# Kernel tuning notes

Hardware: AMD Instinct MI355X
Metric: run time of the kernel (lower is better)

Reference implementation:

```python
import jax, jax.numpy as jnp
import numpy as np

B = 65536
QUERY_DIM = 1024
CROSS_DIM = 1024
HEADS = 16
DIM_HEAD = 64
INNER = HEADS * DIM_HEAD  # 1024
SCALE = DIM_HEAD ** -0.5


def setup_inputs() -> dict:
    key = jax.random.key(0)
    ks = jax.random.split(key, 7)
    s_in = 1.0 / np.sqrt(QUERY_DIM)
    s_c = 1.0 / np.sqrt(CROSS_DIM)
    s_o = 1.0 / np.sqrt(INNER)
    return {
        "latent": jax.random.normal(ks[0], (B, QUERY_DIM), jnp.float32),
        "cond_latent": jax.random.normal(ks[1], (B, CROSS_DIM), jnp.float32),
        "Wq": jax.random.normal(ks[2], (INNER, QUERY_DIM), jnp.float32) * s_in,
        "Wk": jax.random.normal(ks[3], (INNER, CROSS_DIM), jnp.float32) * s_c,
        "Wv": jax.random.normal(ks[4], (INNER, CROSS_DIM), jnp.float32) * s_c,
        "Wout": jax.random.normal(ks[5], (QUERY_DIM, INNER), jnp.float32) * s_o,
        "bout": jax.random.normal(ks[6], (QUERY_DIM,), jnp.float32) * s_o,
    }


def reference(latent, cond_latent, Wq, Wk, Wv, Wout, bout):
    # projections: [B, inner] -> [B, heads, dim_head]
    Q = (latent @ Wq.T).reshape(B, HEADS, DIM_HEAD)
    K = (cond_latent @ Wk.T).reshape(B, HEADS, DIM_HEAD)
    V = (cond_latent @ Wv.T).reshape(B, HEADS, DIM_HEAD)
    # attention across the heads axis: scores [B, heads, heads]
    scores = jnp.einsum("bhd,bgd->bhg", Q, K) * SCALE
    probs = jax.nn.softmax(scores, axis=-1)
    feats = jnp.einsum("bhg,bgd->bhd", probs, V).reshape(B, INNER)
    return feats @ Wout.T + bout
```

## Files before the change

### kernel.cpp

```cpp
#include <hip/hip_runtime.h>
#include <hip/hip_bf16.h>

#define NB    65536
#define KDIM  1024
#define NDIM  1024

#define BM 256
#define BN 256
#define BK 32
#define NT (KDIM / BK)

typedef float f32x4 __attribute__((ext_vector_type(4)));
typedef short short8 __attribute__((ext_vector_type(8)));
typedef unsigned short ushort8v __attribute__((ext_vector_type(8)));

static __device__ __forceinline__ unsigned short f2bf(float f) {
    union { float f; unsigned u; } v; v.f = f;
    unsigned r = v.u + 0x7FFFu + ((v.u >> 16) & 1u);
    return (unsigned short)(r >> 16);
}
static __device__ __forceinline__ float bf2f(unsigned short h) {
    union { unsigned u; float f; } v; v.u = ((unsigned)h) << 16;
    return v.f;
}

static __device__ __forceinline__ void gload16(const unsigned short* g, unsigned short* l) {
    __builtin_amdgcn_global_load_lds(
        (const __attribute__((address_space(1))) unsigned int*)g,
        (__attribute__((address_space(3))) unsigned int*)l, 16, 0, 0);
}

__global__ __launch_bounds__(256) void f32_to_bf16_k(
    const float* __restrict__ s, unsigned short* __restrict__ d, int n4)
{
    const int stride = gridDim.x * 256;
    for (int i = blockIdx.x * 256 + threadIdx.x; i < n4; i += stride) {
        float4 v = reinterpret_cast<const float4*>(s)[i];
        ushort4 o;
        o.x = f2bf(v.x); o.y = f2bf(v.y); o.z = f2bf(v.z); o.w = f2bf(v.w);
        reinterpret_cast<ushort4*>(d)[i] = o;
    }
}

template<int OUT_F32>
__global__ __launch_bounds__(512, 2) void gemm256(
    const unsigned short* __restrict__ Ap, const unsigned short* __restrict__ Wp,
    const float* __restrict__ bias, void* __restrict__ Cptr)
{
    constexpr int N = NDIM;
    constexpr int GN = NDIM / BN;
    __shared__ alignas(16) unsigned short lds[4][2][16][512];

    const int t    = threadIdx.x;
    const int lane = t & 63;
    const int wid  = t >> 6;
    const int wm   = wid >> 2;
    const int wn   = wid & 3;

    const int nwg  = gridDim.x;
    const int cpx  = nwg >> 3;
    const int orig = blockIdx.x;
    const int wgid = (orig & 7) * cpx + (orig >> 3);
    const int bn0  = (wgid & (GN - 1)) * BN;
    const int bm0  = (wgid / GN) * BM;

    const size_t aoff = (size_t)(lane & 15) * KDIM + (lane >> 4) * 8;

#define LDA_(S, MI) \
    (*reinterpret_cast<const short8*>(&lds[S][0][wm * 8 + (MI)][lane * 8]))
#define LDB_(S, NI) \
    (*reinterpret_cast<const short8*>(&lds[S][1][wn * 4 + (NI)][lane * 8]))

#define STAGE_(TAU, SLOT) do {                                                  \
        int _tc = (TAU) < NT ? (TAU) : NT - 1;                  \
        _Pragma("unroll")                                                       \
        for (int _ab = 0; _ab < 2; ++_ab) {                                     \
            const unsigned short* _b = _ab ? Wp : Ap;                           \
            int _r0 = _ab ? bn0 : bm0;                                          \
            _Pragma("unroll")                                                   \
            for (int _j = 0; _j < 2; ++_j) {                                    \
                int _f = wid * 2 + _j;                                          \
                gload16(_b + (size_t)(_r0 + _f * 16) * KDIM + _tc * BK + aoff,  \
                        &lds[SLOT][_ab][_f][0]);                                \
            }                                                                   \
        }                                                                       \
    } while (0)

    f32x4 acc[8][4];
#pragma unroll
    for (int mi = 0; mi < 8; ++mi)
#pragma unroll
        for (int ni = 0; ni < 4; ++ni)
            acc[mi][ni] = (f32x4){0.f, 0.f, 0.f, 0.f};

    STAGE_(0, 0); STAGE_(1, 1); STAGE_(2, 2);

#pragma unroll 1
    for (int tt = 0; tt < NT; ++tt) {
        const int slot = tt & 3;
        STAGE_(tt + 3, (tt + 3) & 3);
        asm volatile("s_waitcnt vmcnt(12)" ::: "memory");
        __builtin_amdgcn_s_barrier();

        short8 af[8], bq[4];
#pragma unroll
        for (int mi = 0; mi < 8; ++mi) af[mi] = LDA_(slot, mi);
#pragma unroll
        for (int ni = 0; ni < 4; ++ni) bq[ni] = LDB_(slot, ni);
        __builtin_amdgcn_s_setprio(1);
#pragma unroll
        for (int mi = 0; mi < 8; ++mi)
#pragma unroll
            for (int ni = 0; ni < 4; ++ni)
                acc[mi][ni] = __builtin_amdgcn_mfma_f32_16x16x32_bf16(
                    af[mi], bq[ni], acc[mi][ni], 0, 0, 0);
        __builtin_amdgcn_s_setprio(0);
        __builtin_amdgcn_s_barrier();
    }

    asm volatile("s_waitcnt vmcnt(0)" ::: "memory");
    __builtin_amdgcn_s_barrier();

    const int crow = (lane >> 4) * 4;
    const int ccol = lane & 15;

    if (OUT_F32) {
        float* Cf = (float*)Cptr;
        float* bbf = reinterpret_cast<float*>(&lds[0][0][0][0]);
        float bv[4];
#pragma unroll
        for (int ni = 0; ni < 4; ++ni)
            bv[ni] = bias[bn0 + wn * 64 + ni * 16 + ccol];
#pragma unroll
        for (int p = 0; p < 4; ++p) {
            if (wm == (p >> 1)) {
#pragma unroll
                for (int ml = 0; ml < 4; ++ml)
#pragma unroll
                    for (int ni = 0; ni < 4; ++ni)
#pragma unroll
                        for (int r = 0; r < 4; ++r)
                            bbf[(ml * 16 + crow + r) * 268 + wn * 64 + ni * 16 + ccol]
                                = acc[(p & 1) * 4 + ml][ni][r] + bv[ni];
            }
            __syncthreads();
#pragma unroll
            for (int it = 0; it < 8; ++it) {
                int lrow = wid * 8 + it;
                f32x4 v = *reinterpret_cast<const f32x4*>(&bbf[lrow * 268 + lane * 4]);
                *reinterpret_cast<f32x4*>(
                    &Cf[(size_t)(bm0 + p * 64 + lrow) * N + bn0 + lane * 4]) = v;
            }
            __syncthreads();
        }
    } else {
        unsigned short* Cb = (unsigned short*)Cptr;
        unsigned short* bb = &lds[0][0][0][0];
#pragma unroll
        for (int p = 0; p < 2; ++p) {
            if (wm == p) {
#pragma unroll
                for (int ml = 0; ml < 8; ++ml)
#pragma unroll
                    for (int ni = 0; ni < 4; ++ni)
#pragma unroll
                        for (int r = 0; r < 4; ++r)
                            bb[(ml * 16 + crow + r) * 264 + wn * 64 + ni * 16 + ccol]
                                = f2bf(acc[ml][ni][r]);
            }
            __syncthreads();
#pragma unroll
            for (int it = 0; it < 8; ++it) {
                int lrow = wid * 16 + it * 2 + (lane >> 5);
                int lcol = (lane & 31) * 8;
                ushort8v v = *reinterpret_cast<const ushort8v*>(&bb[lrow * 264 + lcol]);
                *reinterpret_cast<ushort8v*>(
                    &Cb[(size_t)(bm0 + p * 128 + lrow) * N + bn0 + lcol]) = v;
            }
            __syncthreads();
        }
    }
#undef LDA_
#undef LDB_
#undef STAGE_
}

__global__ __launch_bounds__(256) void attn_k(
    const unsigned short* __restrict__ Qb, const unsigned short* __restrict__ Kb,
    const unsigned short* __restrict__ Vb, unsigned short* __restrict__ Fb)
{
    __shared__ alignas(16) unsigned short KL[4][1024];
    __shared__ alignas(16) unsigned short VL[4][1024];
    const int t = threadIdx.x;
    const int lane = t & 63;
    const int wid = t >> 6;
    const size_t row = (size_t)blockIdx.x * 4 + wid;
    const size_t base = row * 1024;
    const int off = lane * 16;

    ushort8v q0 = *reinterpret_cast<const ushort8v*>(&Qb[base + off]);
    ushort8v q1 = *reinterpret_cast<const ushort8v*>(&Qb[base + off + 8]);
    float qf[16];
#pragma unroll
    for (int j = 0; j < 8; ++j) { qf[j] = bf2f(q0[j]); qf[8 + j] = bf2f(q1[j]); }

    *reinterpret_cast<ushort8v*>(&KL[wid][off])     = *reinterpret_cast<const ushort8v*>(&Kb[base + off]);
    *reinterpret_cast<ushort8v*>(&KL[wid][off + 8]) = *reinterpret_cast<const ushort8v*>(&Kb[base + off + 8]);
    *reinterpret_cast<ushort8v*>(&VL[wid][off])     = *reinterpret_cast<const ushort8v*>(&Vb[base + off]);
    *reinterpret_cast<ushort8v*>(&VL[wid][off + 8]) = *reinterpret_cast<const ushort8v*>(&Vb[base + off + 8]);
    __syncthreads();

    const int sub = lane & 3;
    float s[16];
#pragma unroll
    for (int g = 0; g < 16; ++g) {
        const ushort8v k0 = *reinterpret_cast<const ushort8v*>(&KL[wid][g * 64 + sub * 16]);
        const ushort8v k1 = *reinterpret_cast<const ushort8v*>(&KL[wid][g * 64 + sub * 16 + 8]);
        float acc = 0.f;
#pragma unroll
        for (int j = 0; j < 8; ++j)
            acc += qf[j] * bf2f(k0[j]) + qf[8 + j] * bf2f(k1[j]);
        s[g] = acc;
    }
#pragma unroll
    for (int m = 1; m <= 2; m <<= 1)
#pragma unroll
        for (int g = 0; g < 16; ++g)
            s[g] += __shfl_xor(s[g], m, 64);

    float mx = s[0];
#pragma unroll
    for (int g = 1; g < 16; ++g) mx = fmaxf(mx, s[g]);
    float p[16], denom = 0.f;
#pragma unroll
    for (int g = 0; g < 16; ++g) {
        p[g] = __expf((s[g] - mx) * 0.125f);
        denom += p[g];
    }
    float inv = 1.f / denom;

    float f[16];
#pragma unroll
    for (int j = 0; j < 16; ++j) f[j] = 0.f;
#pragma unroll
    for (int g = 0; g < 16; ++g) {
        float pg = p[g] * inv;
        const ushort8v v0 = *reinterpret_cast<const ushort8v*>(&VL[wid][g * 64 + sub * 16]);
        const ushort8v v1 = *reinterpret_cast<const ushort8v*>(&VL[wid][g * 64 + sub * 16 + 8]);
#pragma unroll
        for (int j = 0; j < 8; ++j) {
            f[j]     += pg * bf2f(v0[j]);
            f[8 + j] += pg * bf2f(v1[j]);
        }
    }
    ushort8v o0, o1;
#pragma unroll
    for (int j = 0; j < 8; ++j) { o0[j] = f2bf(f[j]); o1[j] = f2bf(f[8 + j]); }
    *reinterpret_cast<ushort8v*>(&Fb[base + off])     = o0;
    *reinterpret_cast<ushort8v*>(&Fb[base + off + 8]) = o1;
}

extern "C" void kernel_launch(void* const* d_in, const int* in_sizes, int n_in,
                              void* d_out, int out_size, void* d_ws, size_t ws_size,
                              hipStream_t stream)
{
    (void)in_sizes; (void)n_in; (void)out_size; (void)ws_size;
    const float* latent = (const float*)d_in[0];
    const float* cond   = (const float*)d_in[1];
    const float* Wq     = (const float*)d_in[2];
    const float* Wk     = (const float*)d_in[3];
    const float* Wv     = (const float*)d_in[4];
    const float* Wout   = (const float*)d_in[5];
    const float* bout   = (const float*)d_in[6];
    float* out = (float*)d_out;

    char* ws = (char*)d_ws;
    const size_t MB = 1ull << 20;
    unsigned short* wqb = (unsigned short*)(ws + 0 * MB);
    unsigned short* wkb = (unsigned short*)(ws + 2 * MB);
    unsigned short* wvb = (unsigned short*)(ws + 4 * MB);
    unsigned short* wob = (unsigned short*)(ws + 6 * MB);
    unsigned short* Qb  = (unsigned short*)(ws + 8 * MB);
    unsigned short* Kbf = (unsigned short*)(ws + 8 * MB + 128 * MB);
    unsigned short* Vbf = (unsigned short*)(ws + 8 * MB + 256 * MB);
    unsigned short* Lb  = (unsigned short*)(ws + 8 * MB + 384 * MB);
    unsigned short* Cb  = (unsigned short*)(ws + 8 * MB + 512 * MB);

    const int wn4 = (KDIM * NDIM) / 4;
    f32_to_bf16_k<<<1024, 256, 0, stream>>>(Wq,   wqb, wn4);
    f32_to_bf16_k<<<1024, 256, 0, stream>>>(Wk,   wkb, wn4);
    f32_to_bf16_k<<<1024, 256, 0, stream>>>(Wv,   wvb, wn4);
    f32_to_bf16_k<<<1024, 256, 0, stream>>>(Wout, wob, wn4);

    const int an4 = (NB * KDIM) / 4;
    f32_to_bf16_k<<<4096, 256, 0, stream>>>(latent, Lb, an4);
    f32_to_bf16_k<<<4096, 256, 0, stream>>>(cond,   Cb, an4);

    const int nblk = (NB / BM) * (NDIM / BN);
    gemm256<0><<<nblk, 512, 0, stream>>>(Lb, wqb, nullptr, Qb);
    gemm256<0><<<nblk, 512, 0, stream>>>(Cb, wkb, nullptr, Kbf);
    gemm256<0><<<nblk, 512, 0, stream>>>(Cb, wvb, nullptr, Vbf);

    attn_k<<<NB / 4, 256, 0, stream>>>(Qb, Kbf, Vbf, Qb);

    gemm256<1><<<nblk, 512, 0, stream>>>(Qb, wob, bout, out);
}
```

Measured before the change: 1.028 ms.

## Double-buffer LDS fragment reads to overlap with MFMA in bf16 GEMM

New measurement: 1.033 ms. No clear change (+0.5%).

```diff
diff --git a/kernel.cpp b/kernel.cpp
--- a/kernel.cpp
+++ b/kernel.cpp
@@ -66,10 +66,16 @@
 
     const size_t aoff = (size_t)(lane & 15) * KDIM + (lane >> 4) * 8;
 
-#define LDA_(S, MI) \
-    (*reinterpret_cast<const short8*>(&lds[S][0][wm * 8 + (MI)][lane * 8]))
-#define LDB_(S, NI) \
-    (*reinterpret_cast<const short8*>(&lds[S][1][wn * 4 + (NI)][lane * 8]))
+#define READS_(S, AF, BQ) do {                                                  \
+        _Pragma("unroll")                                                       \
+        for (int _mi = 0; _mi < 8; ++_mi)                                       \
+            AF[_mi] = *reinterpret_cast<const short8*>(                         \
+                &lds[S][0][wm * 8 + _mi][lane * 8]);                            \
+        _Pragma("unroll")                                                       \
+        for (int _ni = 0; _ni < 4; ++_ni)                                       \
+            BQ[_ni] = *reinterpret_cast<const short8*>(                         \
+                &lds[S][1][wn * 4 + _ni][lane * 8]);                            \
+    } while (0)
 
 #define STAGE_(TAU, SLOT) do {                                                  \
         int _tc = (TAU) < NT ? (TAU) : NT - 1;                  \
@@ -86,6 +92,17 @@
         }                                                                       \
     } while (0)
 
+#define MFMA_(AF, BQ) do {                                                      \
+        __builtin_amdgcn_s_setprio(1);                                          \
+        _Pragma("unroll")                                                       \
+        for (int _mi = 0; _mi < 8; ++_mi)                                       \
+            _Pragma("unroll")                                                   \
+            for (int _ni = 0; _ni < 4; ++_ni)                                   \
+                acc[_mi][_ni] = __builtin_amdgcn_mfma_f32_16x16x32_bf16(        \
+                    AF[_mi], BQ[_ni], acc[_mi][_ni], 0, 0, 0);                  \
+        __builtin_amdgcn_s_setprio(0);                                          \
+    } while (0)
+
     f32x4 acc[8][4];
 #pragma unroll
     for (int mi = 0; mi < 8; ++mi)
@@ -93,28 +110,25 @@
         for (int ni = 0; ni < 4; ++ni)
             acc[mi][ni] = (f32x4){0.f, 0.f, 0.f, 0.f};
 
+    short8 afA[8], bqA[4], afB[8], bqB[4];
+
     STAGE_(0, 0); STAGE_(1, 1); STAGE_(2, 2);
+    asm volatile("s_waitcnt vmcnt(4)" ::: "memory");
+    __builtin_amdgcn_s_barrier();
+    READS_(0, afA, bqA);
 
 #pragma unroll 1
-    for (int tt = 0; tt < NT; ++tt) {
-        const int slot = tt & 3;
+    for (int tt = 0; tt < NT; tt += 2) {
+        READS_((tt + 1) & 3, afB, bqB);
         STAGE_(tt + 3, (tt + 3) & 3);
-        asm volatile("s_waitcnt vmcnt(12)" ::: "memory");
+        MFMA_(afA, bqA);
+        asm volatile("s_waitcnt vmcnt(4)" ::: "memory");
         __builtin_amdgcn_s_barrier();
 
-        short8 af[8], bq[4];
-#pragma unroll
-        for (int mi = 0; mi < 8; ++mi) af[mi] = LDA_(slot, mi);
-#pragma unroll
-        for (int ni = 0; ni < 4; ++ni) bq[ni] = LDB_(slot, ni);
-        __builtin_amdgcn_s_setprio(1);
-#pragma unroll
-        for (int mi = 0; mi < 8; ++mi)
-#pragma unroll
-            for (int ni = 0; ni < 4; ++ni)
-                acc[mi][ni] = __builtin_amdgcn_mfma_f32_16x16x32_bf16(
-                    af[mi], bq[ni], acc[mi][ni], 0, 0, 0);
-        __builtin_amdgcn_s_setprio(0);
+        if (tt + 2 < NT) READS_((tt + 2) & 3, afA, bqA);
+        STAGE_(tt + 4, (tt + 4) & 3);
+        MFMA_(afB, bqB);
+        asm volatile("s_waitcnt vmcnt(4)" ::: "memory");
         __builtin_amdgcn_s_barrier();
     }
 
@@ -180,9 +194,9 @@
             __syncthreads();
         }
     }
-#undef LDA_
-#undef LDB_
+#undef READS_
 #undef STAGE_
+#undef MFMA_
 }
 
 __global__ __launch_bounds__(256) void attn_k(
```

## Pre-pack operands into MFMA tile layout and fuse K/V projection GEMMs

Applied to the files above, without the earlier changes.

Measured after the change: 1.013 ms. About the same (-1.5%).

```diff
diff --git a/kernel.cpp b/kernel.cpp
--- a/kernel.cpp
+++ b/kernel.cpp
@@ -10,7 +10,7 @@
 #define BK 32
 #define NT (KDIM / BK)
 
-typedef float f32x4 __attribute__((ext_vector_type(4)));
+typedef float f32x4  __attribute__((ext_vector_type(4)));
 typedef short short8 __attribute__((ext_vector_type(8)));
 typedef unsigned short ushort8v __attribute__((ext_vector_type(8)));
 
@@ -30,25 +30,38 @@
         (__attribute__((address_space(3))) unsigned int*)l, 16, 0, 0);
 }
 
-__global__ __launch_bounds__(256) void f32_to_bf16_k(
-    const float* __restrict__ s, unsigned short* __restrict__ d, int n4)
+
+__global__ __launch_bounds__(256) void pack_f32_k(
+    const float* __restrict__ src, unsigned short* __restrict__ dst)
 {
-    const int stride = gridDim.x * 256;
-    for (int i = blockIdx.x * 256 + threadIdx.x; i < n4; i += stride) {
-        float4 v = reinterpret_cast<const float4*>(s)[i];
-        ushort4 o;
-        o.x = f2bf(v.x); o.y = f2bf(v.y); o.z = f2bf(v.z); o.w = f2bf(v.w);
-        reinterpret_cast<ushort4*>(d)[i] = o;
-    }
-}
-
-template<int OUT_F32>
+    const int tid = threadIdx.x;
+    const int r   = blockIdx.x * 16 + (tid >> 4);
+    const int cb  = (tid & 15) * 64;
+    const int p   = r >> 8;
+    const int f   = (r >> 4) & 15;
+    const int rl  = r & 15;
+    const float* s = src + (size_t)r * 1024 + cb;
+#pragma unroll
+    for (int g = 0; g < 8; ++g) {
+        float4 va = *reinterpret_cast<const float4*>(s + g * 8);
+        float4 vb = *reinterpret_cast<const float4*>(s + g * 8 + 4);
+        ushort8v o;
+        o[0] = f2bf(va.x); o[1] = f2bf(va.y); o[2] = f2bf(va.z); o[3] = f2bf(va.w);
+        o[4] = f2bf(vb.x); o[5] = f2bf(vb.y); o[6] = f2bf(vb.z); o[7] = f2bf(vb.w);
+        const int c0 = cb + g * 8;
+        const int t  = c0 >> 5;
+        const int kc = (c0 & 31) >> 3;
+        *reinterpret_cast<ushort8v*>(
+            &dst[((size_t)(p * 32 + t) * 16 + f) * 512 + kc * 128 + rl * 8]) = o;
+    }
+}
+
+template<int OUT_F32, int NN>
 __global__ __launch_bounds__(512, 2) void gemm256(
     const unsigned short* __restrict__ Ap, const unsigned short* __restrict__ Wp,
     const float* __restrict__ bias, void* __restrict__ Cptr)
 {
-    constexpr int N = NDIM;
-    constexpr int GN = NDIM / BN;
+    constexpr int GN = NN / BN;
     __shared__ alignas(16) unsigned short lds[4][2][16][512];
 
     const int t    = threadIdx.x;
@@ -64,23 +77,19 @@
     const int bn0  = (wgid & (GN - 1)) * BN;
     const int bm0  = (wgid / GN) * BM;
 
-    const size_t aoff = (size_t)(lane & 15) * KDIM + (lane >> 4) * 8;
-
-#define LDA_(S, MI) \
-    (*reinterpret_cast<const short8*>(&lds[S][0][wm * 8 + (MI)][lane * 8]))
-#define LDB_(S, NI) \
-    (*reinterpret_cast<const short8*>(&lds[S][1][wn * 4 + (NI)][lane * 8]))
+    const int pA = bm0 >> 8;
+    const int pB = bn0 >> 8;
 
 #define STAGE_(TAU, SLOT) do {                                                  \
-        int _tc = (TAU) < NT ? (TAU) : NT - 1;                  \
+        int _tc = (TAU) < NT ? (TAU) : NT - 1;                                  \
         _Pragma("unroll")                                                       \
         for (int _ab = 0; _ab < 2; ++_ab) {                                     \
             const unsigned short* _b = _ab ? Wp : Ap;                           \
-            int _r0 = _ab ? bn0 : bm0;                                          \
+            int _pp = _ab ? pB : pA;                                            \
             _Pragma("unroll")                                                   \
             for (int _j = 0; _j < 2; ++_j) {                                    \
                 int _f = wid * 2 + _j;                                          \
-                gload16(_b + (size_t)(_r0 + _f * 16) * KDIM + _tc * BK + aoff,  \
+                gload16(_b + ((size_t)(_pp * 32 + _tc) * 16 + _f) * 512 + lane * 8, \
                         &lds[SLOT][_ab][_f][0]);                                \
             }                                                                   \
         }                                                                       \
@@ -104,9 +113,11 @@
 
         short8 af[8], bq[4];
 #pragma unroll
-        for (int mi = 0; mi < 8; ++mi) af[mi] = LDA_(slot, mi);
-#pragma unroll
-        for (int ni = 0; ni < 4; ++ni) bq[ni] = LDB_(slot, ni);
+        for (int mi = 0; mi < 8; ++mi)
+            af[mi] = *reinterpret_cast<const short8*>(&lds[slot][0][wm * 8 + mi][lane * 8]);
+#pragma unroll
+        for (int ni = 0; ni < 4; ++ni)
+            bq[ni] = *reinterpret_cast<const short8*>(&lds[slot][1][wn * 4 + ni][lane * 8]);
         __builtin_amdgcn_s_setprio(1);
 #pragma unroll
         for (int mi = 0; mi < 8; ++mi)
@@ -117,13 +128,11 @@
         __builtin_amdgcn_s_setprio(0);
         __builtin_amdgcn_s_barrier();
     }
-
     asm volatile("s_waitcnt vmcnt(0)" ::: "memory");
     __builtin_amdgcn_s_barrier();
 
     const int crow = (lane >> 4) * 4;
     const int ccol = lane & 15;
-
     if (OUT_F32) {
         float* Cf = (float*)Cptr;
         float* bbf = reinterpret_cast<float*>(&lds[0][0][0][0]);
@@ -149,7 +158,7 @@
                 int lrow = wid * 8 + it;
                 f32x4 v = *reinterpret_cast<const f32x4*>(&bbf[lrow * 268 + lane * 4]);
                 *reinterpret_cast<f32x4*>(
-                    &Cf[(size_t)(bm0 + p * 64 + lrow) * N + bn0 + lane * 4]) = v;
+                    &Cf[(size_t)(bm0 + p * 64 + lrow) * NN + bn0 + lane * 4]) = v;
             }
             __syncthreads();
         }
@@ -175,27 +184,26 @@
                 int lcol = (lane & 31) * 8;
                 ushort8v v = *reinterpret_cast<const ushort8v*>(&bb[lrow * 264 + lcol]);
                 *reinterpret_cast<ushort8v*>(
-                    &Cb[(size_t)(bm0 + p * 128 + lrow) * N + bn0 + lcol]) = v;
+                    &Cb[(size_t)(bm0 + p * 128 + lrow) * NN + bn0 + lcol]) = v;
             }
             __syncthreads();
         }
     }
-#undef LDA_
-#undef LDB_
 #undef STAGE_
 }
 
-__global__ __launch_bounds__(256) void attn_k(
-    const unsigned short* __restrict__ Qb, const unsigned short* __restrict__ Kb,
-    const unsigned short* __restrict__ Vb, unsigned short* __restrict__ Fb)
+__global__ __launch_bounds__(1024) void attn_k(
+    const unsigned short* __restrict__ Qb, const unsigned short* __restrict__ KVb,
+    unsigned short* __restrict__ Fp)
 {
-    __shared__ alignas(16) unsigned short KL[4][1024];
-    __shared__ alignas(16) unsigned short VL[4][1024];
+    __shared__ alignas(16) unsigned short KL[16][1024];
+    __shared__ alignas(16) unsigned short VL[16][1024];
     const int t = threadIdx.x;
     const int lane = t & 63;
     const int wid = t >> 6;
-    const size_t row = (size_t)blockIdx.x * 4 + wid;
+    const size_t row = (size_t)blockIdx.x * 16 + wid;
     const size_t base = row * 1024;
+    const size_t bkv  = row * 2048;
     const int off = lane * 16;
 
     ushort8v q0 = *reinterpret_cast<const ushort8v*>(&Qb[base + off]);
@@ -204,10 +212,10 @@
 #pragma unroll
     for (int j = 0; j < 8; ++j) { qf[j] = bf2f(q0[j]); qf[8 + j] = bf2f(q1[j]); }
 
-    *reinterpret_cast<ushort8v*>(&KL[wid][off])     = *reinterpret_cast<const ushort8v*>(&Kb[base + off]);
-    *reinterpret_cast<ushort8v*>(&KL[wid][off + 8]) = *reinterpret_cast<const ushort8v*>(&Kb[base + off + 8]);
-    *reinterpret_cast<ushort8v*>(&VL[wid][off])     = *reinterpret_cast<const ushort8v*>(&Vb[base + off]);
-    *reinterpret_cast<ushort8v*>(&VL[wid][off + 8]) = *reinterpret_cast<const ushort8v*>(&Vb[base + off + 8]);
+    *reinterpret_cast<ushort8v*>(&KL[wid][off])     = *reinterpret_cast<const ushort8v*>(&KVb[bkv + off]);
+    *reinterpret_cast<ushort8v*>(&KL[wid][off + 8]) = *reinterpret_cast<const ushort8v*>(&KVb[bkv + off + 8]);
+    *reinterpret_cast<ushort8v*>(&VL[wid][off])     = *reinterpret_cast<const ushort8v*>(&KVb[bkv + 1024 + off]);
+    *reinterpret_cast<ushort8v*>(&VL[wid][off + 8]) = *reinterpret_cast<const ushort8v*>(&KVb[bkv + 1024 + off + 8]);
     __syncthreads();
 
     const int sub = lane & 3;
@@ -256,8 +264,19 @@
     ushort8v o0, o1;
 #pragma unroll
     for (int j = 0; j < 8; ++j) { o0[j] = f2bf(f[j]); o1[j] = f2bf(f[8 + j]); }
-    *reinterpret_cast<ushort8v*>(&Fb[base + off])     = o0;
-    *reinterpret_cast<ushort8v*>(&Fb[base + off + 8]) = o1;
+    *reinterpret_cast<ushort8v*>(&KL[wid][off])     = o0;
+    *reinterpret_cast<ushort8v*>(&KL[wid][off + 8]) = o1;
+    __syncthreads();
+
+    const int r0 = blockIdx.x * 16;
+    const int pp = r0 >> 8;
+    const int ff = (r0 >> 4) & 15;
+    const int tt = t >> 5;
+    const int kc = (t >> 3) & 3;
+    const int rp = t & 7;
+    unsigned short* db = &Fp[((size_t)(pp * 32 + tt) * 16 + ff) * 512 + kc * 128 + rp * 16];
+    *reinterpret_cast<ushort8v*>(db)     = *reinterpret_cast<const ushort8v*>(&KL[rp * 2][tt * 32 + kc * 8]);
+    *reinterpret_cast<ushort8v*>(db + 8) = *reinterpret_cast<const ushort8v*>(&KL[rp * 2 + 1][tt * 32 + kc * 8]);
 }
 
 extern "C" void kernel_launch(void* const* d_in, const int* in_sizes, int n_in,
@@ -276,32 +295,27 @@
 
     char* ws = (char*)d_ws;
     const size_t MB = 1ull << 20;
-    unsigned short* wqb = (unsigned short*)(ws + 0 * MB);
-    unsigned short* wkb = (unsigned short*)(ws + 2 * MB);
-    unsigned short* wvb = (unsigned short*)(ws + 4 * MB);
-    unsigned short* wob = (unsigned short*)(ws + 6 * MB);
-    unsigned short* Qb  = (unsigned short*)(ws + 8 * MB);
-    unsigned short* Kbf = (unsigned short*)(ws + 8 * MB + 128 * MB);
-    unsigned short* Vbf = (unsigned short*)(ws + 8 * MB + 256 * MB);
-    unsigned short* Lb  = (unsigned short*)(ws + 8 * MB + 384 * MB);
-    unsigned short* Cb  = (unsigned short*)(ws + 8 * MB + 512 * MB);
-
-    const int wn4 = (KDIM * NDIM) / 4;
-    f32_to_bf16_k<<<1024, 256, 0, stream>>>(Wq,   wqb, wn4);
-    f32_to_bf16_k<<<1024, 256, 0, stream>>>(Wk,   wkb, wn4);
-    f32_to_bf16_k<<<1024, 256, 0, stream>>>(Wv,   wvb, wn4);
-    f32_to_bf16_k<<<1024, 256, 0, stream>>>(Wout, wob, wn4);
-
-    const int an4 = (NB * KDIM) / 4;
-    f32_to_bf16_k<<<4096, 256, 0, stream>>>(latent, Lb, an4);
-    f32_to_bf16_k<<<4096, 256, 0, stream>>>(cond,   Cb, an4);
-
-    const int nblk = (NB / BM) * (NDIM / BN);
-    gemm256<0><<<nblk, 512, 0, stream>>>(Lb, wqb, nullptr, Qb);
-    gemm256<0><<<nblk, 512, 0, stream>>>(Cb, wkb, nullptr, Kbf);
-    gemm256<0><<<nblk, 512, 0, stream>>>(Cb, wvb, nullptr, Vbf);
-
-    attn_k<<<NB / 4, 256, 0, stream>>>(Qb, Kbf, Vbf, Qb);
-
-    gemm256<1><<<nblk, 512, 0, stream>>>(Qb, wob, bout, out);
-}
+    unsigned short* wqp  = (unsigned short*)(ws + 0 * MB);
+    unsigned short* wkvp = (unsigned short*)(ws + 2 * MB);
+    unsigned short* wop  = (unsigned short*)(ws + 6 * MB);
+    unsigned short* Qb   = (unsigned short*)(ws + 8 * MB);
+    unsigned short* KVb  = (unsigned short*)(ws + 136 * MB);
+    unsigned short* Lp   = (unsigned short*)(ws + 392 * MB);
+    unsigned short* Cp   = (unsigned short*)(ws + 520 * MB);
+    unsigned short* Fp   = Lp;
+
+    pack_f32_k<<<NDIM / 16, 256, 0, stream>>>(Wq,   wqp);
+    pack_f32_k<<<NDIM / 16, 256, 0, stream>>>(Wk,   wkvp);
+    pack_f32_k<<<NDIM / 16, 256, 0, stream>>>(Wv,   wkvp + 1048576);
+    pack_f32_k<<<NDIM / 16, 256, 0, stream>>>(Wout, wop);
+
+    pack_f32_k<<<NB / 16, 256, 0, stream>>>(latent, Lp);
+    pack_f32_k<<<NB / 16, 256, 0, stream>>>(cond,   Cp);
+
+    gemm256<0, 1024><<<1024, 512, 0, stream>>>(Lp, wqp,  nullptr, Qb);
+    gemm256<0, 2048><<<2048, 512, 0, stream>>>(Cp, wkvp, nullptr, KVb);
+
+    attn_k<<<NB / 16, 1024, 0, stream>>>(Qb, KVb, Fp);
+
+    gemm256<1, 1024><<<1024, 512, 0, stream>>>(Fp, wop, bout, out);
+}
```
